# Kernel tuning notes

Measured on AMD Instinct MI355X. Metric: run time of the kernel, lower is better.

Reference implementation:

```python
import jax, jax.numpy as jnp
import numpy as np

N_AGENTS = 262144
GRID = 1024
C = 8
HIDDEN = 64
DT = 0.1
SENSOR_ANGLE = 0.6
SENSOR_LEN = 3.0
DECAY = 0.99


def setup_inputs() -> dict:
    key = jax.random.key(0)
    k1, k2, k3, k4, k5 = jax.random.split(key, 5)
    agent_pos = jax.random.uniform(k1, (2, N_AGENTS), minval=2.0, maxval=GRID - 2.0, dtype=jnp.float32)
    agent_vel = jax.random.uniform(k2, (2, N_AGENTS), minval=-1.0, maxval=1.0, dtype=jnp.float32)
    pheremone_lattice = jax.random.uniform(k3, (C, GRID, GRID), dtype=jnp.float32)
    W1 = jax.random.normal(k4, (3 * C, HIDDEN), dtype=jnp.float32) * 0.1
    b1 = jnp.zeros((HIDDEN,), dtype=jnp.float32)
    W2 = jax.random.normal(k5, (HIDDEN, 2 + C), dtype=jnp.float32) * 0.1
    b2 = jnp.zeros((2 + C,), dtype=jnp.float32)
    return {"agent_pos": agent_pos, "agent_vel": agent_vel, "pheremone_lattice": pheremone_lattice,
            "W1": W1, "b1": b1, "W2": W2, "b2": b2}


def _sense(agent_pos, agent_vel, lattice):
    # heading angle per agent, 3 sensor offsets: 0, +a, -a
    theta = jnp.arctan2(agent_vel[1], agent_vel[0])                      # [N]
    offs = jnp.array([0.0, SENSOR_ANGLE, -SENSOR_ANGLE], dtype=agent_pos.dtype)
    ang = theta[None, :] + offs[:, None]                                  # [3,N]
    cx = jnp.rint(agent_pos[0][None, :] + SENSOR_LEN * jnp.cos(ang)).astype(jnp.int32)  # [3,N]
    cy = jnp.rint(agent_pos[1][None, :] + SENSOR_LEN * jnp.sin(ang)).astype(jnp.int32)
    d = jnp.array([-1, 0, 1], dtype=jnp.int32)
    xi = (cx[:, :, None] + d) % GRID                                      # [3,N,3]
    yi = (cy[:, :, None] + d) % GRID
    # Cartesian product of x and y offsets (meshgrid in original) -> 3x3 window
    X = xi[:, :, :, None]                                                 # [3,N,3,1]
    Y = yi[:, :, None, :]                                                 # [3,N,1,3]
    vals = lattice[:, X, Y]                                               # [C,3,N,3,3]
    w = vals.sum(axis=(-1, -2))                                           # [C,3,N]
    return w[:, 0].T, w[:, 1].T, w[:, 2].T                                # each [N,C]


def reference(agent_pos, agent_vel, pheremone_lattice, W1, b1, W2, b2):
    w_front, w_left, w_right = _sense(agent_pos, agent_vel, pheremone_lattice)
    # per-agent MLP (vmapped agent_nn in original): concat 3 sensor readings
    x = jnp.concatenate([w_front, w_left, w_right], axis=-1)              # [N,3C]
    h = jnp.tanh(x @ W1 + b1)                                             # [N,HIDDEN]
    o = h @ W2 + b2                                                       # [N,2+C]
    new_vel = o[:, :2].T                                                  # [2,N]
    d_pher = o[:, 2:].T                                                   # [C,N]
    # deposit pheremones at rounded agent positions (scatter-set, relu clamp)
    pos_i = jnp.rint(agent_pos).astype(jnp.int32)                         # [2,N]
    cur = pheremone_lattice[:, pos_i[0], pos_i[1]]                        # [C,N]
    lat = pheremone_lattice.at[:, pos_i[0], pos_i[1]].set(jax.nn.relu(cur + DT * d_pher))
    # gaussian_blur == 0 -> diffusion is identity; then decay
    lat = lat * DECAY
    # periodic position update
    new_pos = (agent_pos + new_vel * DT) % GRID
    return (new_pos, new_vel, lat)
```

## Files before the change

### kernel.cpp

```cpp
#include <hip/hip_runtime.h>
#include <hip/hip_bf16.h>
#include <math.h>

#define GRIDN 1024
#define NAGENTS 262144
#define CCH 8
#define HIDDEN 64
#define DT 0.1f
#define DECAYF 0.99f
#define SENSOR_LEN 3.0f
#define COS_SA 0.82533561490967829724f
#define SIN_SA 0.56464247339503535720f

typedef __attribute__((ext_vector_type(8))) short short8;

__device__ __forceinline__ float fast_tanh(float x) {
    float xc = fminf(fmaxf(x, -9.0f), 9.0f);
    float t = __builtin_amdgcn_exp2f(xc * 2.88539008177792681472f);
    return (t - 1.0f) * __builtin_amdgcn_rcpf(t + 1.0f);
}

__global__ void __launch_bounds__(256) k_winner(const float* __restrict__ pos,
                                                int* __restrict__ winner) {
    int i = blockIdx.x * blockDim.x + threadIdx.x;
    int gx = (int)rintf(pos[i]) & (GRIDN - 1);
    int gy = (int)rintf(pos[i + NAGENTS]) & (GRIDN - 1);
    atomicMax(&winner[(gx << 10) + gy], i);
}

__global__ void __launch_bounds__(256) k_boxT(const float* __restrict__ lat,
                                              __hip_bfloat16* __restrict__ BT,
                                              int* __restrict__ winner) {
    int idx = blockIdx.x * blockDim.x + threadIdx.x;
    winner[idx] = -1;
    int x = idx >> 10, y = idx & (GRIDN - 1);
    int xm = (x + GRIDN - 1) & (GRIDN - 1), xp = (x + 1) & (GRIDN - 1);
    int ym = (y + GRIDN - 1) & (GRIDN - 1), yp = (y + 1) & (GRIDN - 1);
    __hip_bfloat16 out[CCH];
#pragma unroll
    for (int c = 0; c < CCH; ++c) {
        const float* L = lat + (size_t)c * GRIDN * GRIDN;
        const float* r0 = L + xm * GRIDN;
        const float* r1 = L + x * GRIDN;
        const float* r2 = L + xp * GRIDN;
        float s = r0[ym] + r0[y] + r0[yp]
                + r1[ym] + r1[y] + r1[yp]
                + r2[ym] + r2[y] + r2[yp];
        out[c] = __float2bfloat16(s);
    }
    *(short8*)(BT + (size_t)idx * CCH) = *(const short8*)out;
}

__global__ void __launch_bounds__(256) k_agent(
    const float* __restrict__ pos, const float* __restrict__ vel,
    const __hip_bfloat16* __restrict__ BT,
    const float* __restrict__ W1, const float* __restrict__ b1,
    const float* __restrict__ W2, const float* __restrict__ b2,
    float* __restrict__ out_pos, float* __restrict__ out_vel,
    float* __restrict__ dp) {
    int i = blockIdx.x * blockDim.x + threadIdx.x;
    float px = pos[i], py = pos[i + NAGENTS];
    float vx = vel[i], vy = vel[i + NAGENTS];

    float r2 = vx * vx + vy * vy;
    float ct, st;
    if (r2 > 0.f) {
        float inv = rsqrtf(r2);
        ct = vx * inv;
        st = vy * inv;
    } else {
        ct = 1.f;
        st = 0.f;
    }

    float dirx[3], diry[3];
    dirx[0] = ct;                          diry[0] = st;
    dirx[1] = ct * COS_SA - st * SIN_SA;   diry[1] = st * COS_SA + ct * SIN_SA;
    dirx[2] = ct * COS_SA + st * SIN_SA;   diry[2] = st * COS_SA - ct * SIN_SA;

    short8 raw[3];
#pragma unroll
    for (int s = 0; s < 3; ++s) {
        int gx = ((int)rintf(px + SENSOR_LEN * dirx[s]) + GRIDN) & (GRIDN - 1);
        int gy = ((int)rintf(py + SENSOR_LEN * diry[s]) + GRIDN) & (GRIDN - 1);
        raw[s] = *(const short8*)(BT + ((size_t)(gx << 10) + gy) * CCH);
    }

    float xin[3 * CCH];
#pragma unroll
    for (int s = 0; s < 3; ++s)
#pragma unroll
        for (int c = 0; c < CCH; ++c) {
            unsigned u = ((unsigned)(unsigned short)raw[s][c]) << 16;
            xin[s * CCH + c] = __builtin_bit_cast(float, u);
        }

    float h[HIDDEN];
#pragma unroll
    for (int j = 0; j < HIDDEN; ++j) h[j] = b1[j];
    for (int ii = 0; ii < 3 * CCH; ++ii) {
        float xi = xin[ii];
        const float* w = W1 + ii * HIDDEN;
#pragma unroll
        for (int j = 0; j < HIDDEN; ++j) h[j] = fmaf(xi, w[j], h[j]);
    }

    float o[2 + CCH];
#pragma unroll
    for (int k = 0; k < 2 + CCH; ++k) o[k] = b2[k];
    for (int j = 0; j < HIDDEN; ++j) {
        float t = fast_tanh(h[j]);
        const float* w2 = W2 + j * (2 + CCH);
#pragma unroll
        for (int k = 0; k < 2 + CCH; ++k) o[k] = fmaf(t, w2[k], o[k]);
    }

    float nvx = o[0], nvy = o[1];
    float npx = px + nvx * DT;
    if (npx >= (float)GRIDN) npx -= (float)GRIDN;
    if (npx < 0.f) npx += (float)GRIDN;
    float npy = py + nvy * DT;
    if (npy >= (float)GRIDN) npy -= (float)GRIDN;
    if (npy < 0.f) npy += (float)GRIDN;

    out_pos[i] = npx;
    out_pos[i + NAGENTS] = npy;
    out_vel[i] = nvx;
    out_vel[i + NAGENTS] = nvy;

    float4* dpp = (float4*)(dp + (size_t)i * CCH);
    dpp[0] = make_float4(o[2], o[3], o[4], o[5]);
    dpp[1] = make_float4(o[6], o[7], o[8], o[9]);
}

__global__ void __launch_bounds__(256) k_update(const float* __restrict__ lat,
                                                const int* __restrict__ winner,
                                                const float* __restrict__ dp,
                                                float* __restrict__ out_lat) {
    int idx = blockIdx.x * blockDim.x + threadIdx.x;
    int w = winner[idx];
    float d[CCH];
    if (w >= 0) {
        const float4* dpp = (const float4*)(dp + (size_t)w * CCH);
        float4 a = dpp[0], b = dpp[1];
        d[0] = a.x; d[1] = a.y; d[2] = a.z; d[3] = a.w;
        d[4] = b.x; d[5] = b.y; d[6] = b.z; d[7] = b.w;
    }
#pragma unroll
    for (int c = 0; c < CCH; ++c) {
        size_t off = (size_t)c * GRIDN * GRIDN + idx;
        float v = lat[off];
        if (w >= 0) v = fmaxf(v + DT * d[c], 0.f);
        out_lat[off] = v * DECAYF;
    }
}

extern "C" void kernel_launch(void* const* d_in, const int* in_sizes, int n_in,
                              void* d_out, int out_size, void* d_ws, size_t ws_size,
                              hipStream_t stream) {
    const float* pos = (const float*)d_in[0];
    const float* vel = (const float*)d_in[1];
    const float* lat = (const float*)d_in[2];
    const float* W1  = (const float*)d_in[3];
    const float* b1  = (const float*)d_in[4];
    const float* W2  = (const float*)d_in[5];
    const float* b2  = (const float*)d_in[6];

    float* out      = (float*)d_out;
    float* out_pos  = out;
    float* out_vel  = out + 2 * NAGENTS;
    float* out_lat  = out + 4 * NAGENTS;

    char* ws = (char*)d_ws;
    int*            winner = (int*)ws;
    float*          dp     = (float*)(ws + (4 << 20));
    __hip_bfloat16* BT     = (__hip_bfloat16*)(ws + (12 << 20));

    const int ncell = GRIDN * GRIDN;

    k_boxT<<<ncell / 256, 256, 0, stream>>>(lat, BT, winner);
    k_winner<<<NAGENTS / 256, 256, 0, stream>>>(pos, winner);
    k_agent<<<NAGENTS / 256, 256, 0, stream>>>(pos, vel, BT, W1, b1, W2, b2,
                                               out_pos, out_vel, dp);
    k_update<<<ncell / 256, 256, 0, stream>>>(lat, winner, dp, out_lat);
}
```

Measured before the change: 74.42 us.

## Split each agent's MLP across four lanes and fold winner scatter into agent kernel

Each agent is now handled by four lanes. Each lane gathers one sensor window, and the windows are exchanged with shuffles. Each lane then computes 16 of the 64 hidden units and a partial output, and the partials are reduced with xor-shuffles. This cuts per-thread register pressure and serial FMA chains to raise occupancy and parallelism. The separate winner atomicMax kernel is folded into the fourth lane, which saves a launch and re-reading the positions. The cost is four times as many threads, redundant position and velocity loads per lane, and shuffle overhead.

```diff
diff --git a/kernel.cpp b/kernel.cpp
--- a/kernel.cpp
+++ b/kernel.cpp
@@ -20,12 +20,11 @@
     return (t - 1.0f) * __builtin_amdgcn_rcpf(t + 1.0f);
 }
 
-__global__ void __launch_bounds__(256) k_winner(const float* __restrict__ pos,
-                                                int* __restrict__ winner) {
-    int i = blockIdx.x * blockDim.x + threadIdx.x;
-    int gx = (int)rintf(pos[i]) & (GRIDN - 1);
-    int gy = (int)rintf(pos[i + NAGENTS]) & (GRIDN - 1);
-    atomicMax(&winner[(gx << 10) + gy], i);
+__device__ __forceinline__ float bf16_lo(unsigned u) {
+    return __builtin_bit_cast(float, u << 16);
+}
+__device__ __forceinline__ float bf16_hi(unsigned u) {
+    return __builtin_bit_cast(float, u & 0xffff0000u);
 }
 
 __global__ void __launch_bounds__(256) k_boxT(const float* __restrict__ lat,
@@ -57,8 +56,11 @@
     const float* __restrict__ W1, const float* __restrict__ b1,
     const float* __restrict__ W2, const float* __restrict__ b2,
     float* __restrict__ out_pos, float* __restrict__ out_vel,
-    float* __restrict__ dp) {
-    int i = blockIdx.x * blockDim.x + threadIdx.x;
+    float* __restrict__ dp, int* __restrict__ winner) {
+    int tid = blockIdx.x * blockDim.x + threadIdx.x;
+    int i = tid >> 2;
+    int t = tid & 3;
+
     float px = pos[i], py = pos[i + NAGENTS];
     float vx = vel[i], vy = vel[i + NAGENTS];
 
@@ -73,64 +75,85 @@
         st = 0.f;
     }
 
-    float dirx[3], diry[3];
-    dirx[0] = ct;                          diry[0] = st;
-    dirx[1] = ct * COS_SA - st * SIN_SA;   diry[1] = st * COS_SA + ct * SIN_SA;
-    dirx[2] = ct * COS_SA + st * SIN_SA;   diry[2] = st * COS_SA - ct * SIN_SA;
-
-    short8 raw[3];
+    float dx, dy;
+    if (t == 1)      { dx = ct * COS_SA - st * SIN_SA; dy = st * COS_SA + ct * SIN_SA; }
+    else if (t == 2) { dx = ct * COS_SA + st * SIN_SA; dy = st * COS_SA - ct * SIN_SA; }
+    else             { dx = ct;                        dy = st; }
+
+    int gx = ((int)rintf(px + SENSOR_LEN * dx) + GRIDN) & (GRIDN - 1);
+    int gy = ((int)rintf(py + SENSOR_LEN * dy) + GRIDN) & (GRIDN - 1);
+    uint4 u = *(const uint4*)(BT + ((size_t)(gx << 10) + gy) * CCH);
+
+    unsigned xk[12];
 #pragma unroll
     for (int s = 0; s < 3; ++s) {
-        int gx = ((int)rintf(px + SENSOR_LEN * dirx[s]) + GRIDN) & (GRIDN - 1);
-        int gy = ((int)rintf(py + SENSOR_LEN * diry[s]) + GRIDN) & (GRIDN - 1);
-        raw[s] = *(const short8*)(BT + ((size_t)(gx << 10) + gy) * CCH);
-    }
-
-    float xin[3 * CCH];
-#pragma unroll
-    for (int s = 0; s < 3; ++s)
-#pragma unroll
-        for (int c = 0; c < CCH; ++c) {
-            unsigned u = ((unsigned)(unsigned short)raw[s][c]) << 16;
-            xin[s * CCH + c] = __builtin_bit_cast(float, u);
+        xk[s * 4 + 0] = __shfl(u.x, s, 4);
+        xk[s * 4 + 1] = __shfl(u.y, s, 4);
+        xk[s * 4 + 2] = __shfl(u.z, s, 4);
+        xk[s * 4 + 3] = __shfl(u.w, s, 4);
+    }
+
+    float h[16];
+    const float4* b1v = (const float4*)(b1 + t * 16);
+#pragma unroll
+    for (int q = 0; q < 4; ++q) {
+        float4 b = b1v[q];
+        h[q * 4 + 0] = b.x; h[q * 4 + 1] = b.y;
+        h[q * 4 + 2] = b.z; h[q * 4 + 3] = b.w;
+    }
+#pragma unroll
+    for (int k = 0; k < 3 * CCH; ++k) {
+        float xv = (k & 1) ? bf16_hi(xk[k >> 1]) : bf16_lo(xk[k >> 1]);
+        const float4* wr = (const float4*)(W1 + k * HIDDEN + t * 16);
+#pragma unroll
+        for (int q = 0; q < 4; ++q) {
+            float4 w = wr[q];
+            h[q * 4 + 0] = fmaf(xv, w.x, h[q * 4 + 0]);
+            h[q * 4 + 1] = fmaf(xv, w.y, h[q * 4 + 1]);
+            h[q * 4 + 2] = fmaf(xv, w.z, h[q * 4 + 2]);
+            h[q * 4 + 3] = fmaf(xv, w.w, h[q * 4 + 3]);
         }
-
-    float h[HIDDEN];
-#pragma unroll
-    for (int j = 0; j < HIDDEN; ++j) h[j] = b1[j];
-    for (int ii = 0; ii < 3 * CCH; ++ii) {
-        float xi = xin[ii];
-        const float* w = W1 + ii * HIDDEN;
-#pragma unroll
-        for (int j = 0; j < HIDDEN; ++j) h[j] = fmaf(xi, w[j], h[j]);
     }
 
     float o[2 + CCH];
 #pragma unroll
-    for (int k = 0; k < 2 + CCH; ++k) o[k] = b2[k];
-    for (int j = 0; j < HIDDEN; ++j) {
-        float t = fast_tanh(h[j]);
-        const float* w2 = W2 + j * (2 + CCH);
-#pragma unroll
-        for (int k = 0; k < 2 + CCH; ++k) o[k] = fmaf(t, w2[k], o[k]);
-    }
-
-    float nvx = o[0], nvy = o[1];
-    float npx = px + nvx * DT;
-    if (npx >= (float)GRIDN) npx -= (float)GRIDN;
-    if (npx < 0.f) npx += (float)GRIDN;
-    float npy = py + nvy * DT;
-    if (npy >= (float)GRIDN) npy -= (float)GRIDN;
-    if (npy < 0.f) npy += (float)GRIDN;
-
-    out_pos[i] = npx;
-    out_pos[i + NAGENTS] = npy;
-    out_vel[i] = nvx;
-    out_vel[i + NAGENTS] = nvy;
-
-    float4* dpp = (float4*)(dp + (size_t)i * CCH);
-    dpp[0] = make_float4(o[2], o[3], o[4], o[5]);
-    dpp[1] = make_float4(o[6], o[7], o[8], o[9]);
+    for (int k = 0; k < 2 + CCH; ++k) o[k] = 0.f;
+#pragma unroll
+    for (int jj = 0; jj < 16; ++jj) {
+        float tj = fast_tanh(h[jj]);
+        const float* w2 = W2 + (t * 16 + jj) * (2 + CCH);
+#pragma unroll
+        for (int k = 0; k < 2 + CCH; ++k) o[k] = fmaf(tj, w2[k], o[k]);
+    }
+
+#pragma unroll
+    for (int k = 0; k < 2 + CCH; ++k) {
+        o[k] += __shfl_xor(o[k], 1, 4);
+        o[k] += __shfl_xor(o[k], 2, 4);
+        o[k] += b2[k];
+    }
+
+    if (t == 0) {
+        float nvx = o[0], nvy = o[1];
+        float npx = px + nvx * DT;
+        if (npx >= (float)GRIDN) npx -= (float)GRIDN;
+        if (npx < 0.f) npx += (float)GRIDN;
+        float npy = py + nvy * DT;
+        if (npy >= (float)GRIDN) npy -= (float)GRIDN;
+        if (npy < 0.f) npy += (float)GRIDN;
+        out_pos[i] = npx;
+        out_pos[i + NAGENTS] = npy;
+        out_vel[i] = nvx;
+        out_vel[i + NAGENTS] = nvy;
+    } else if (t == 1) {
+        *(float4*)(dp + (size_t)i * CCH) = make_float4(o[2], o[3], o[4], o[5]);
+    } else if (t == 2) {
+        *(float4*)(dp + (size_t)i * CCH + 4) = make_float4(o[6], o[7], o[8], o[9]);
+    } else {
+        int wx = (int)rintf(px) & (GRIDN - 1);
+        int wy = (int)rintf(py) & (GRIDN - 1);
+        atomicMax(&winner[(wx << 10) + wy], i);
+    }
 }
 
 __global__ void __launch_bounds__(256) k_update(const float* __restrict__ lat,
@@ -179,8 +202,7 @@
     const int ncell = GRIDN * GRIDN;
 
     k_boxT<<<ncell / 256, 256, 0, stream>>>(lat, BT, winner);
-    k_winner<<<NAGENTS / 256, 256, 0, stream>>>(pos, winner);
-    k_agent<<<NAGENTS / 256, 256, 0, stream>>>(pos, vel, BT, W1, b1, W2, b2,
-                                               out_pos, out_vel, dp);
+    k_agent<<<NAGENTS * 4 / 256, 256, 0, stream>>>(pos, vel, BT, W1, b1, W2, b2,
+                                                   out_pos, out_vel, dp, winner);
     k_update<<<ncell / 256, 256, 0, stream>>>(lat, winner, dp, out_lat);
 }
```

Result: slower. 198.2 us (+166.4%).
